# Performance work log

Measured on AMD Instinct MI355X. Metric: run time of the kernel, lower is better.

The kernel has to match this reference:

```python
import jax, jax.numpy as jnp
import numpy as np

B = 16384        # batch size
D = 128          # embedding dim == ln_bot[-1]
N_EMB = 26       # number of sparse tables
VOCAB = 50000    # rows per table
LN_BOT = [13, 512, 256, 128]
LN_TOP = [479, 1024, 1024, 512, 1]
# triangular indices matching: li=[i for i in range(ni) for j in range(i)] (offset=0, no self-interaction)
LI, LJ = np.tril_indices(N_EMB + 1, -1)


def _init_linear(key, n_in, n_out):
    kw, kb = jax.random.split(key)
    lim = 1.0 / np.sqrt(n_in)
    W = jax.random.uniform(kw, (n_in, n_out), minval=-lim, maxval=lim, dtype=jnp.float32)
    b = jax.random.uniform(kb, (n_out,), minval=-lim, maxval=lim, dtype=jnp.float32)
    return W, b


def setup_inputs() -> dict:
    key = jax.random.key(0)
    ks = jax.random.split(key, 3 + len(LN_BOT) - 1 + len(LN_TOP) - 1)
    inp = {
        "dense_x": jax.random.normal(ks[0], (B, LN_BOT[0]), dtype=jnp.float32),
        "indices": jax.random.randint(ks[1], (N_EMB, B), 0, VOCAB),
        "emb_tables": jax.random.normal(ks[2], (N_EMB, VOCAB, D), dtype=jnp.float32) * 0.01,
    }
    k = 3
    for i in range(len(LN_BOT) - 1):
        W, b = _init_linear(ks[k], LN_BOT[i], LN_BOT[i + 1]); k += 1
        inp[f"bot_W{i}"], inp[f"bot_b{i}"] = W, b
    for i in range(len(LN_TOP) - 1):
        W, b = _init_linear(ks[k], LN_TOP[i], LN_TOP[i + 1]); k += 1
        inp[f"top_W{i}"], inp[f"top_b{i}"] = W, b
    return inp


def reference(dense_x, indices, emb_tables,
              bot_W0, bot_b0, bot_W1, bot_b1, bot_W2, bot_b2,
              top_W0, top_b0, top_W1, top_b1, top_W2, top_b2, top_W3, top_b3):
    # bottom MLP (sigmoid_bot=-1 -> all ReLU)
    x = dense_x
    for W, b in ((bot_W0, bot_b0), (bot_W1, bot_b1), (bot_W2, bot_b2)):
        x = jax.nn.relu(x @ W + b)                      # [B, 128]

    # embedding lookups (bag size 1 per table)
    emb = jax.vmap(lambda t, i: t[i])(emb_tables, indices)   # [26, B, D]
    emb = jnp.transpose(emb, (1, 0, 2))                      # [B, 26, D]

    # dot interaction
    T = jnp.concatenate([x[:, None, :], emb], axis=1)        # [B, 27, D]
    Z = jnp.einsum('bid,bjd->bij', T, T)                     # [B, 27, 27]
    Zflat = Z[:, LI, LJ]                                     # [B, 351]
    R = jnp.concatenate([x, Zflat], axis=1)                  # [B, 479]

    # top MLP (sigmoid on last layer, sigmoid_top=3)
    h = R
    for W, b in ((top_W0, top_b0), (top_W1, top_b1), (top_W2, top_b2)):
        h = jax.nn.relu(h @ W + b)
    p = jax.nn.sigmoid(h @ top_W3 + top_b3)                  # [B, 1]
    return jnp.clip(p, 0.0, 1.0)                             # loss_threshold = 0.0
```

## Files before the change

### kernel.cpp

```cpp
#include <hip/hip_runtime.h>

typedef __attribute__((ext_vector_type(8))) short short8;
typedef __attribute__((ext_vector_type(4))) float f32x4;
typedef __attribute__((ext_vector_type(16))) float f32x16;

#define B_ROWS 16384

__device__ __forceinline__ float bf2f(ushort u){ return __uint_as_float(((uint)u)<<16); }
__device__ __forceinline__ ushort f2bf(float f){
  uint u = __float_as_uint(f);
  u = u + 0x7FFFu + ((u>>16)&1u);
  return (ushort)(u>>16);
}
__device__ __forceinline__ void gload_lds16(const void* g, void* l){
  __builtin_amdgcn_global_load_lds((const __attribute__((address_space(1))) unsigned*)g,
                                   (__attribute__((address_space(3))) unsigned*)l, 16, 0, 0);
}

struct TArgs { const float* in; ushort* out; int K, N, Kp; };
struct PrepArgs {
  const float* x; const float* W0; const float* b0; ushort* act0;
  TArgs t[5];
  float* partial;
};

__global__ __launch_bounds__(256) void prep(PrepArgs a)
{
  const int idx = blockIdx.x;
  const int tid = threadIdx.x;
  __shared__ float tile[32][33];

  if (idx < 32768){
    int i = idx*256 + tid;
    int b = i>>9, n = i&511;
    const float* xr = a.x + (size_t)b*13;
    float s = a.b0[n];
    #pragma unroll
    for (int k=0;k<13;k++) s += xr[k]*a.W0[k*512+n];
    a.act0[i] = f2bf(fmaxf(s,0.f));
    return;
  }
  if (idx >= 34976){
    a.partial[(idx-34976)*256 + tid] = 0.f;
    return;
  }
  int t = idx - 32768, s, kx, ny;
  if (t < 128)              { s=0; kx=t&15; ny=t>>4; }
  else if ((t-=128) < 32)   { s=1; kx=t&7 ; ny=t>>3; }
  else if ((t-=32) < 512)   { s=2; kx=t&15; ny=t>>4; }
  else if ((t-=512) < 1024) { s=3; kx=t&31; ny=t>>5; }
  else { t-=1024;             s=4; kx=t&31; ny=t>>5; }
  TArgs ta = a.t[s];
  int k0 = kx*32, n0 = ny*32;
  const int c = tid & 31, r8 = tid >> 5;
  #pragma unroll
  for (int p=0;p<4;p++){
    int k = k0 + r8 + p*8;
    tile[r8+p*8][c] = (k < ta.K) ? ta.in[(size_t)k*ta.N + n0 + c] : 0.f;
  }
  __syncthreads();
  #pragma unroll
  for (int p=0;p<4;p++){
    int n = n0 + r8 + p*8;
    ta.out[(size_t)n*ta.Kp + k0 + c] = f2bf(tile[c][r8+p*8]);
  }
}

template<int TM, bool RELU>
__global__ __launch_bounds__(256) void gemm_bt(const ushort* __restrict__ A,
    const ushort* __restrict__ Bt, const float* __restrict__ bias,
    ushort* __restrict__ C, int M, int N, int K, int ldc)
{
  constexpr int BM = TM*32;
  __shared__ __align__(16) ushort lA[2][BM*64];
  __shared__ __align__(16) ushort lB[2][128*64];
  const int tid = threadIdx.x;
  const int wave = tid>>6, lane = tid&63;
  const int bm = blockIdx.x*BM, bn = blockIdx.y*128;
  const int wrr = (wave>>1)*(BM/2), wcc = (wave&1)*64;
  const int lr = lane&15, lg = lane>>4;
  const int nt = K>>6;
  const int obA = wave*(TM*1024) + lane*16;
  const int obB = wave*4096 + lane*16;

  f32x4 acc[TM][4];
  #pragma unroll
  for (int m=0;m<TM;m++)
    #pragma unroll
    for (int n=0;n<4;n++)
      #pragma unroll
      for (int j=0;j<4;j++) acc[m][n][j] = 0.f;

  auto stage = [&](int buf, int kt){
    #pragma unroll
    for (int c=0;c<TM;c++){
      int o = obA + c*1024;
      int row = o>>7, colb = o&127;
      gload_lds16((const char*)A  + (((size_t)(bm+row)*K + (kt<<6))<<1) + colb, (char*)lA[buf] + o);
    }
    #pragma unroll
    for (int c=0;c<4;c++){
      int o = obB + c*1024;
      int row = o>>7, colb = o&127;
      gload_lds16((const char*)Bt + (((size_t)(bn+row)*K + (kt<<6))<<1) + colb, (char*)lB[buf] + o);
    }
  };

  stage(0, 0);
  int cur = 0;
  for (int t=0; t<nt; ++t){
    int nx = (t+1 < nt) ? t+1 : 0;
    stage(cur^1, nx);
    if constexpr (TM==4) asm volatile("s_waitcnt vmcnt(8)" ::: "memory");
    else                 asm volatile("s_waitcnt vmcnt(6)" ::: "memory");
    __builtin_amdgcn_s_barrier();
    asm volatile("" ::: "memory");
    #pragma unroll
    for (int kk=0;kk<64;kk+=32){
      short8 af[TM], bfr[4];
      const int lk = kk + lg*8;
      #pragma unroll
      for (int m=0;m<TM;m++) af[m]  = *(const short8*)&lA[cur][(wrr+m*16+lr)*64 + lk];
      #pragma unroll
      for (int n=0;n<4;n++) bfr[n] = *(const short8*)&lB[cur][(wcc+n*16+lr)*64 + lk];
      #pragma unroll
      for (int m=0;m<TM;m++)
        #pragma unroll
        for (int n=0;n<4;n++)
          acc[m][n] = __builtin_amdgcn_mfma_f32_16x16x32_bf16(af[m], bfr[n], acc[m][n], 0,0,0);
    }
    asm volatile("" ::: "memory");
    __builtin_amdgcn_s_barrier();
    cur ^= 1;
  }

  #pragma unroll
  for (int n=0;n<4;n++){
    int col = bn + wcc + n*16 + lr;
    float bv = bias[col];
    #pragma unroll
    for (int m=0;m<TM;m++){
      #pragma unroll
      for (int j=0;j<4;j++){
        int row = bm + wrr + m*16 + lg*4 + j;
        float v = acc[m][n][j] + bv;
        if (RELU) v = fmaxf(v,0.f);
        C[(size_t)row*ldc + col] = f2bf(v);
      }
    }
  }
}

template<int BN, bool FUSE>
__global__ __launch_bounds__(512, 2) void gemm256(const ushort* __restrict__ A,
    const ushort* __restrict__ Bt, const float* __restrict__ bias,
    ushort* __restrict__ C, int K, int ldc,
    const float* __restrict__ w3, float* __restrict__ partial)
{
  constexpr int  NF = BN/128;
  constexpr int  LB = BN/128;
  constexpr uint BR = (uint)BN*32u;
  constexpr uint BUFSZ = 16384u + 2u*BR;
  __shared__ __align__(16) ushort lds[2*BUFSZ];

  const int tid = threadIdx.x;
  const int wave = tid>>6, lane = tid&63;
  const uint wm = (uint)(wave>>2), wn = (uint)(wave&3);
  const uint lc = (uint)(lane&31), hi = (uint)(lane>>5);

  const uint nwg = gridDim.x*gridDim.y;
  const uint flat = blockIdx.y*gridDim.x + blockIdx.x;
  const uint cpx = nwg >> 3;
  const uint swz = (flat & 7u)*cpx + (flat >> 3);
  const int bm = (int)(swz % gridDim.x)*256, bn = (int)(swz / gridDim.x)*BN;

  const int nt = K>>6, niter = nt>>1;

  f32x16 acc[4][NF];
  #pragma unroll
  for (int m=0;m<4;m++)
    #pragma unroll
    for (int n=0;n<NF;n++)
      #pragma unroll
      for (int j=0;j<16;j++) acc[m][n][j] = 0.f;

  short8 bfr[2][NF];

#define STAGE(MAT, KH, TILE, SBUF) do{                                          \
    int kt_ = (TILE);                                                           \
    int ktc_ = (kt_ < nt) ? kt_ : 0;                                            \
    const ushort* gb_ = (MAT) ? Bt : A;                                         \
    const uint ro_ = (MAT) ? (uint)bn : (uint)bm;                               \
    const uint rb_ = (uint)(SBUF)*BUFSZ + ((MAT) ? (16384u + (uint)(KH)*BR)     \
                                                 : ((uint)(KH)*8192u));         \
    const int nl_ = (MAT) ? LB : 2;                                             \
    _Pragma("unroll")                                                           \
    for (int j_=0; j_<nl_; ++j_){                                               \
      uint lin_ = (uint)tid*16u + (uint)j_*8192u;                               \
      uint src_ = lin_ ^ (((lin_>>7)&3u)<<4);                                   \
      uint row_ = src_>>6, colb_ = src_&63u;                                    \
      const char* g_ = (const char*)gb_ +                                       \
        (((size_t)(ro_+row_)*(size_t)K + (size_t)ktc_*64 + (KH)*32)<<1) + colb_;\
      gload_lds16(g_, (char*)lds + (size_t)rb_*2 + lin_);                       \
    }                                                                           \
  }while(0)

#define PHASE(CBUF, KKH, MH, BLOAD, SMAT, SKH, STILE, SBUF, CKPT) do{           \
    const uint ab_ = (uint)(CBUF)*BUFSZ + (uint)(KKH)*8192u;                    \
    short8 af_[2][2];                                                           \
    _Pragma("unroll")                                                           \
    for (int mfl_=0; mfl_<2; ++mfl_){                                           \
      uint r_ = wm*128u + ((uint)(MH)*2u+(uint)mfl_)*32u + lc;                  \
      _Pragma("unroll")                                                         \
      for (int k2_=0; k2_<2; ++k2_){                                            \
        uint l_ = r_*64u + hi*16u + (uint)k2_*32u;                              \
        af_[mfl_][k2_] = *(const short8*)((const char*)lds + (size_t)ab_*2      \
                                   + (l_ ^ (((l_>>7)&3u)<<4)));                 \
      }                                                                         \
    }                                                                           \
    if (BLOAD){                                                                 \
      const uint bb_ = (uint)(CBUF)*BUFSZ + 16384u + (uint)(KKH)*BR;            \
      _Pragma("unroll")                                                         \
      for (int nf_=0; nf_<NF; ++nf_){                                           \
        uint r_ = wn*(uint)(BN/4) + (uint)nf_*32u + lc;                         \
        _Pragma("unroll")                                                       \
        for (int k2_=0; k2_<2; ++k2_){                                          \
          uint l_ = r_*64u + hi*16u + (uint)k2_*32u;                            \
          bfr[k2_][nf_] = *(const short8*)((const char*)lds + (size_t)bb_*2     \
                                     + (l_ ^ (((l_>>7)&3u)<<4)));               \
        }                                                                       \
      }                                                                         \
    }                                                                           \
    STAGE(SMAT, SKH, STILE, SBUF);                                              \
    asm volatile("" ::: "memory");                                              \
    __builtin_amdgcn_s_barrier();                                               \
    asm volatile("" ::: "memory");                                              \
    __builtin_amdgcn_s_setprio(1);                                              \
    _Pragma("unroll")                                                           \
    for (int mfl_=0; mfl_<2; ++mfl_)                                            \
      _Pragma("unroll")                                                         \
      for (int nf_=0; nf_<NF; ++nf_)                                            \
        _Pragma("unroll")                                                       \
        for (int k2_=0; k2_<2; ++k2_)                                           \
          acc[(MH)*2+mfl_][nf_] = __builtin_amdgcn_mfma_f32_32x32x16_bf16(      \
              af_[mfl_][k2_], bfr[k2_][nf_], acc[(MH)*2+mfl_][nf_], 0,0,0);     \
    __builtin_amdgcn_s_setprio(0);                                              \
    if (CKPT){                                                                  \
      if constexpr (LB==2) asm volatile("s_waitcnt vmcnt(8)" ::: "memory");     \
      else                 asm volatile("s_waitcnt vmcnt(6)" ::: "memory");     \
    }                                                                           \
    asm volatile("" ::: "memory");                                              \
    __builtin_amdgcn_s_barrier();                                               \
  }while(0)

  STAGE(0,0,0,0); STAGE(1,0,0,0); STAGE(0,1,0,0); STAGE(1,1,0,0);
  STAGE(0,0,1,1); STAGE(1,0,1,1);
  if constexpr (LB==2) asm volatile("s_waitcnt vmcnt(4)" ::: "memory");
  else                 asm volatile("s_waitcnt vmcnt(3)" ::: "memory");
  asm volatile("" ::: "memory");
  __builtin_amdgcn_s_barrier();

  for (int i=0; i<niter; ++i){
    const int O  = 2*i+1;
    const int E2 = 2*i+2;
    const int O2 = 2*i+3;
    PHASE(0,0,0,true , 0,1,O ,1, false);
    PHASE(0,0,1,false, 1,1,O ,1, true );
    PHASE(0,1,0,true , 0,0,E2,0, false);
    PHASE(0,1,1,false, 1,0,E2,0, true );
    PHASE(1,0,0,true , 0,1,E2,0, false);
    PHASE(1,0,1,false, 1,1,E2,0, true );
    PHASE(1,1,0,true , 0,0,O2,1, false);
    PHASE(1,1,1,false, 1,0,O2,1, true );
  }
#undef PHASE
#undef STAGE

  if constexpr (FUSE){
    int col = bn + (int)wn*(BN/4) + (int)lc;
    float bv = bias[col];
    float wv = w3[col];
    #pragma unroll
    for (int mf=0; mf<4; ++mf){
      #pragma unroll
      for (int reg=0; reg<16; ++reg){
        float v = fmaxf(acc[mf][0][reg] + bv, 0.f) * wv;
        #pragma unroll
        for (int off=1; off<32; off<<=1) v += __shfl_xor(v, off);
        if (lc == 0){
          int row = bm + (int)wm*128 + mf*32 + (reg&3) + 8*(reg>>2) + 4*(int)hi;
          atomicAdd(&partial[row], v);
        }
      }
    }
  } else {
    #pragma unroll
    for (int nf=0; nf<NF; ++nf){
      int col = bn + (int)wn*(BN/4) + nf*32 + (int)lc;
      float bv = bias[col];
      #pragma unroll
      for (int mf=0; mf<4; ++mf){
        #pragma unroll
        for (int reg=0; reg<16; ++reg){
          int row = bm + (int)wm*128 + mf*32 + (reg&3) + 8*(reg>>2) + 4*(int)hi;
          float v = acc[mf][nf][reg] + bv;
          C[(size_t)row*ldc + col] = f2bf(fmaxf(v, 0.f));
        }
      }
    }
  }
}

__global__ __launch_bounds__(256) void interact(const int* __restrict__ idx,
    const float* __restrict__ emb, ushort* __restrict__ R)
{
  __shared__ __align__(16) ushort Tl[4][32][136];
  const int w = threadIdx.x>>6, l = threadIdx.x&63;
  const int b = blockIdx.x*4 + w;
  ushort* Rrow = R + (size_t)b*512;

  uint xv = ((const uint*)Rrow)[l];
  *(uint*)&Tl[w][0][2*l] = xv;

  int myidx = (l<26) ? idx[(size_t)l*B_ROWS + b] : 0;
  const int half = l>>5, lc = l&31;
  #pragma unroll
  for (int i=0;i<13;i++){
    const int row = 2*i + 1 + half;
    int e = __shfl(myidx, row - 1);
    const float4* rp = (const float4*)(emb + ((size_t)(row-1)*50000 + (size_t)e)*128);
    float4 v = rp[lc];
    uint2 pk;
    pk.x = (uint)f2bf(v.x) | ((uint)f2bf(v.y)<<16);
    pk.y = (uint)f2bf(v.z) | ((uint)f2bf(v.w)<<16);
    *(uint2*)&Tl[w][row][4*lc] = pk;
  }
  __syncthreads();

  f32x16 acc;
  #pragma unroll
  for (int i=0;i<16;i++) acc[i] = 0.f;
  #pragma unroll
  for (int kk=0;kk<8;kk++){
    short8 fa = *(const short8*)((const char*)&Tl[w][0][0] + (size_t)(l&31)*272 + kk*32 + (l>>5)*16);
    acc = __builtin_amdgcn_mfma_f32_32x32x16_bf16(fa, fa, acc, 0,0,0);
  }

  const int c = l&31;
  #pragma unroll
  for (int j=0;j<16;j++){
    int r = (j&3) + 8*(j>>2) + 4*(l>>5);
    if (c < r && r <= 26) Rrow[128 + r*(r-1)/2 + c] = f2bf(acc[j]);
  }
  if (l < 33) Rrow[479 + l] = 0;
}

__global__ __launch_bounds__(256) void sigm(const float* __restrict__ partial,
    const float* __restrict__ b3, float* __restrict__ out)
{
  int i = blockIdx.x*256 + threadIdx.x;
  float h = partial[i] + b3[0];
  float p = 1.f/(1.f + expf(-h));
  out[i] = fminf(fmaxf(p, 0.f), 1.f);
}

extern "C" void kernel_launch(void* const* d_in, const int* in_sizes, int n_in,
                              void* d_out, int out_size, void* d_ws, size_t ws_size,
                              hipStream_t stream)
{
  const float* dense_x = (const float*)d_in[0];
  const int*   indices = (const int*)d_in[1];
  const float* emb     = (const float*)d_in[2];
  const float* bW0 = (const float*)d_in[3];  const float* bb0 = (const float*)d_in[4];
  const float* bW1 = (const float*)d_in[5];  const float* bb1 = (const float*)d_in[6];
  const float* bW2 = (const float*)d_in[7];  const float* bb2 = (const float*)d_in[8];
  const float* tW0 = (const float*)d_in[9];  const float* tb0 = (const float*)d_in[10];
  const float* tW1 = (const float*)d_in[11]; const float* tb1 = (const float*)d_in[12];
  const float* tW2 = (const float*)d_in[13]; const float* tb2 = (const float*)d_in[14];
  const float* tW3 = (const float*)d_in[15]; const float* tb3 = (const float*)d_in[16];
  float* out = (float*)d_out;
  const int Bn = B_ROWS;

  char* ws = (char*)d_ws;
  size_t o = 0;
  auto alloc = [&](size_t bytes)->char*{ char* r = ws + o; o += (bytes + 255) & ~(size_t)255; return r; };
  ushort* wtB1 = (ushort*)alloc(256*512*2);
  ushort* wtB2 = (ushort*)alloc(128*256*2);
  ushort* wtT0 = (ushort*)alloc(1024*512*2);
  ushort* wtT1 = (ushort*)alloc((size_t)1024*1024*2);
  ushort* wtT2 = (ushort*)alloc(512*1024*2);
  float*  partial = (float*)alloc(B_ROWS*4);
  ushort* P    = (ushort*)alloc((size_t)Bn*512*2);
  ushort* act1 = (ushort*)alloc((size_t)Bn*256*2);
  ushort* h1   = (ushort*)alloc((size_t)Bn*1024*2);
  ushort* h2   = (ushort*)alloc((size_t)Bn*1024*2);
  (void)ws_size; (void)in_sizes; (void)n_in; (void)out_size;

  PrepArgs pa;
  pa.x = dense_x; pa.W0 = bW0; pa.b0 = bb0; pa.act0 = P;
  pa.t[0] = { bW1, wtB1, 512 , 256 , 512  };
  pa.t[1] = { bW2, wtB2, 256 , 128 , 256  };
  pa.t[2] = { tW0, wtT0, 479 , 1024, 512  };
  pa.t[3] = { tW1, wtT1, 1024, 1024, 1024 };
  pa.t[4] = { tW2, wtT2, 1024, 512 , 1024 };
  pa.partial = partial;
  prep<<<35040,256,0,stream>>>(pa);

  gemm_bt<4,true><<<dim3(128,2),256,0,stream>>>(P,    wtB1, bb1, act1, Bn,256,512, 256);
  gemm_bt<2,true><<<dim3(256,1),256,0,stream>>>(act1, wtB2, bb2, P,    Bn,128,256, 512);

  interact<<<Bn/4,256,0,stream>>>(indices, emb, P);

  gemm256<256,false><<<dim3(64,4),512,0,stream>>>(P,  wtT0, tb0, h1, 512 , 1024, nullptr, nullptr);
  gemm256<256,false><<<dim3(64,4),512,0,stream>>>(h1, wtT1, tb1, h2, 1024, 1024, nullptr, nullptr);
  gemm256<128,true ><<<dim3(64,4),512,0,stream>>>(h2, wtT2, tb2, nullptr, 1024, 0, tW3, partial);
  sigm<<<Bn/256,256,0,stream>>>(partial, tb3, out);
}
```

Before: 207.7 us.

## Fuse bottom MLP layers 1 and 2 into one kernel keeping activations in LDS

Replaces the two separate bottom-MLP GEMM launches with a single kernel per 64-row tile. It computes layer 1 with the full 256-wide N, stages the ReLU output in LDS, then runs layer 2 against a W2 copy preloaded into LDS. This removes the act1 round trip through global memory and one launch, and adds an XOR swizzle on LDS tiles to avoid bank conflicts. The change also drops the XCD-aware block swizzle from gemm256, which may hurt L2 locality, and the large LDS footprint limits occupancy to one block per CU with only 256 blocks.

```diff
diff --git a/kernel.cpp b/kernel.cpp
--- a/kernel.cpp
+++ b/kernel.cpp
@@ -66,65 +66,75 @@
   }
 }
 
-template<int TM, bool RELU>
-__global__ __launch_bounds__(256) void gemm_bt(const ushort* __restrict__ A,
-    const ushort* __restrict__ Bt, const float* __restrict__ bias,
-    ushort* __restrict__ C, int M, int N, int K, int ldc)
-{
-  constexpr int BM = TM*32;
-  __shared__ __align__(16) ushort lA[2][BM*64];
-  __shared__ __align__(16) ushort lB[2][128*64];
+__global__ __launch_bounds__(256) void bot12(const ushort* __restrict__ act0,
+    const ushort* __restrict__ W1t, const float* __restrict__ b1,
+    const ushort* __restrict__ W2t, const float* __restrict__ b2,
+    ushort* __restrict__ R)
+{
+  __shared__ __align__(16) char smem[147456];
   const int tid = threadIdx.x;
   const int wave = tid>>6, lane = tid&63;
-  const int bm = blockIdx.x*BM, bn = blockIdx.y*128;
-  const int wrr = (wave>>1)*(BM/2), wcc = (wave&1)*64;
   const int lr = lane&15, lg = lane>>4;
-  const int nt = K>>6;
-  const int obA = wave*(TM*1024) + lane*16;
-  const int obB = wave*4096 + lane*16;
-
-  f32x4 acc[TM][4];
-  #pragma unroll
-  for (int m=0;m<TM;m++)
+  const int bm = blockIdx.x*64;
+
+  #pragma unroll
+  for (int j=0;j<16;j++){
+    uint lin = (uint)tid*16u + (uint)j*4096u;
+    gload_lds16((const char*)W2t + (lin ^ (((lin>>9)&7u)<<4)), smem + 81920 + lin);
+  }
+
+  auto stage = [&](int buf, int kt){
+    #pragma unroll
+    for (int c=0;c<2;c++){
+      uint lin = (uint)tid*16u + (uint)c*4096u;
+      uint row = lin>>7, scol = (lin&127u) ^ (((lin>>7)&7u)<<4);
+      gload_lds16((const char*)act0 + (((size_t)(bm+row)*512 + (uint)kt*64u)<<1) + scol,
+                  smem + (buf?8192:0) + lin);
+    }
+    #pragma unroll
+    for (int c=0;c<8;c++){
+      uint lin = (uint)tid*16u + (uint)c*4096u;
+      uint row = lin>>7, scol = (lin&127u) ^ (((lin>>7)&7u)<<4);
+      gload_lds16((const char*)W1t + (((size_t)row*512 + (uint)kt*64u)<<1) + scol,
+                  smem + 16384 + (buf?32768:0) + lin);
+    }
+  };
+
+  f32x4 acc[4][4];
+  #pragma unroll
+  for (int m=0;m<4;m++)
     #pragma unroll
     for (int n=0;n<4;n++)
       #pragma unroll
       for (int j=0;j<4;j++) acc[m][n][j] = 0.f;
 
-  auto stage = [&](int buf, int kt){
-    #pragma unroll
-    for (int c=0;c<TM;c++){
-      int o = obA + c*1024;
-      int row = o>>7, colb = o&127;
-      gload_lds16((const char*)A  + (((size_t)(bm+row)*K + (kt<<6))<<1) + colb, (char*)lA[buf] + o);
-    }
-    #pragma unroll
-    for (int c=0;c<4;c++){
-      int o = obB + c*1024;
-      int row = o>>7, colb = o&127;
-      gload_lds16((const char*)Bt + (((size_t)(bn+row)*K + (kt<<6))<<1) + colb, (char*)lB[buf] + o);
-    }
-  };
-
-  stage(0, 0);
+  stage(0,0);
   int cur = 0;
-  for (int t=0; t<nt; ++t){
-    int nx = (t+1 < nt) ? t+1 : 0;
+  for (int t=0;t<8;t++){
+    int nx = (t+1<8) ? t+1 : 0;
     stage(cur^1, nx);
-    if constexpr (TM==4) asm volatile("s_waitcnt vmcnt(8)" ::: "memory");
-    else                 asm volatile("s_waitcnt vmcnt(6)" ::: "memory");
+    asm volatile("s_waitcnt vmcnt(10)" ::: "memory");
     __builtin_amdgcn_s_barrier();
     asm volatile("" ::: "memory");
-    #pragma unroll
-    for (int kk=0;kk<64;kk+=32){
-      short8 af[TM], bfr[4];
-      const int lk = kk + lg*8;
-      #pragma unroll
-      for (int m=0;m<TM;m++) af[m]  = *(const short8*)&lA[cur][(wrr+m*16+lr)*64 + lk];
-      #pragma unroll
-      for (int n=0;n<4;n++) bfr[n] = *(const short8*)&lB[cur][(wcc+n*16+lr)*64 + lk];
-      #pragma unroll
-      for (int m=0;m<TM;m++)
+    const char* lAc = smem + (cur?8192:0);
+    const char* lBc = smem + 16384 + (cur?32768:0);
+    #pragma unroll
+    for (int kk2=0;kk2<2;kk2++){
+      short8 af[4], bfr[4];
+      #pragma unroll
+      for (int m=0;m<4;m++){
+        uint row = (uint)(m*16+lr);
+        uint l = row*128u + (uint)kk2*64u + (uint)lg*16u;
+        af[m] = *(const short8*)(lAc + (l ^ ((row&7u)<<4)));
+      }
+      #pragma unroll
+      for (int n=0;n<4;n++){
+        uint row = (uint)(wave*64 + n*16+lr);
+        uint l = row*128u + (uint)kk2*64u + (uint)lg*16u;
+        bfr[n] = *(const short8*)(lBc + (l ^ ((row&7u)<<4)));
+      }
+      #pragma unroll
+      for (int m=0;m<4;m++)
         #pragma unroll
         for (int n=0;n<4;n++)
           acc[m][n] = __builtin_amdgcn_mfma_f32_16x16x32_bf16(af[m], bfr[n], acc[m][n], 0,0,0);
@@ -133,21 +143,63 @@
     __builtin_amdgcn_s_barrier();
     cur ^= 1;
   }
-
+  asm volatile("s_waitcnt vmcnt(0)" ::: "memory");
+  __syncthreads();
+
+  ushort* a1 = (ushort*)smem;
   #pragma unroll
   for (int n=0;n<4;n++){
-    int col = bn + wcc + n*16 + lr;
-    float bv = bias[col];
-    #pragma unroll
-    for (int m=0;m<TM;m++){
+    int col = wave*64 + n*16 + lr;
+    float bv = b1[col];
+    #pragma unroll
+    for (int m=0;m<4;m++)
       #pragma unroll
       for (int j=0;j<4;j++){
-        int row = bm + wrr + m*16 + lg*4 + j;
-        float v = acc[m][n][j] + bv;
-        if (RELU) v = fmaxf(v,0.f);
-        C[(size_t)row*ldc + col] = f2bf(v);
-      }
-    }
+        int row = m*16 + lg*4 + j;
+        a1[(uint)row*264u + (uint)col] = f2bf(fmaxf(acc[m][n][j] + bv, 0.f));
+      }
+  }
+  __syncthreads();
+
+  f32x4 acc2[4][2];
+  #pragma unroll
+  for (int m=0;m<4;m++)
+    #pragma unroll
+    for (int n=0;n<2;n++)
+      #pragma unroll
+      for (int j=0;j<4;j++) acc2[m][n][j] = 0.f;
+
+  const char* w2c = smem + 81920;
+  #pragma unroll
+  for (int ks=0;ks<8;ks++){
+    short8 af[4], bw[2];
+    #pragma unroll
+    for (int m=0;m<4;m++)
+      af[m] = *(const short8*)&a1[(uint)(m*16+lr)*264u + (uint)ks*32u + (uint)lg*8u];
+    #pragma unroll
+    for (int n=0;n<2;n++){
+      uint row = (uint)(wave*32 + n*16 + lr);
+      uint l = row*512u + (uint)ks*64u + (uint)lg*16u;
+      bw[n] = *(const short8*)(w2c + (l ^ ((row&7u)<<4)));
+    }
+    #pragma unroll
+    for (int m=0;m<4;m++)
+      #pragma unroll
+      for (int n=0;n<2;n++)
+        acc2[m][n] = __builtin_amdgcn_mfma_f32_16x16x32_bf16(af[m], bw[n], acc2[m][n], 0,0,0);
+  }
+
+  #pragma unroll
+  for (int n=0;n<2;n++){
+    int col = wave*32 + n*16 + lr;
+    float bv = b2[col];
+    #pragma unroll
+    for (int m=0;m<4;m++)
+      #pragma unroll
+      for (int j=0;j<4;j++){
+        int row = bm + m*16 + lg*4 + j;
+        R[(size_t)row*512 + col] = f2bf(fmaxf(acc2[m][n][j] + bv, 0.f));
+      }
   }
 }
 
@@ -167,13 +219,7 @@
   const int wave = tid>>6, lane = tid&63;
   const uint wm = (uint)(wave>>2), wn = (uint)(wave&3);
   const uint lc = (uint)(lane&31), hi = (uint)(lane>>5);
-
-  const uint nwg = gridDim.x*gridDim.y;
-  const uint flat = blockIdx.y*gridDim.x + blockIdx.x;
-  const uint cpx = nwg >> 3;
-  const uint swz = (flat & 7u)*cpx + (flat >> 3);
-  const int bm = (int)(swz % gridDim.x)*256, bn = (int)(swz / gridDim.x)*BN;
-
+  const int bm = blockIdx.x*256, bn = blockIdx.y*BN;
   const int nt = K>>6, niter = nt>>1;
 
   f32x16 acc[4][NF];
@@ -391,7 +437,6 @@
   ushort* wtT2 = (ushort*)alloc(512*1024*2);
   float*  partial = (float*)alloc(B_ROWS*4);
   ushort* P    = (ushort*)alloc((size_t)Bn*512*2);
-  ushort* act1 = (ushort*)alloc((size_t)Bn*256*2);
   ushort* h1   = (ushort*)alloc((size_t)Bn*1024*2);
   ushort* h2   = (ushort*)alloc((size_t)Bn*1024*2);
   (void)ws_size; (void)in_sizes; (void)n_in; (void)out_size;
@@ -406,8 +451,7 @@
   pa.partial = partial;
   prep<<<35040,256,0,stream>>>(pa);
 
-  gemm_bt<4,true><<<dim3(128,2),256,0,stream>>>(P,    wtB1, bb1, act1, Bn,256,512, 256);
-  gemm_bt<2,true><<<dim3(256,1),256,0,stream>>>(act1, wtB2, bb2, P,    Bn,128,256, 512);
+  bot12<<<256,256,0,stream>>>(P, wtB1, bb1, wtB2, bb2, P);
 
   interact<<<Bn/4,256,0,stream>>>(indices, emb, P);
 
```

Result: faster. 184.4 us (-11.2%).
